# Performance work log

Hardware: AMD Instinct MI355X
Metric: run time of the kernel (lower is better)

Reference implementation:

```python
import jax, jax.numpy as jnp
import numpy as np

H = 8          # SD1.4 heads
TAU = 0.1      # HarmCfg.tau
GAMMA = 1.0    # HarmCfg.gamma
EPS = 1e-12    # F.normalize eps


def setup_inputs() -> dict:
    key = jax.random.key(0)
    ks = jax.random.split(key, 8)
    B, S, C, K, D = 16, 4096, 320, 77, 768
    return {
        "hidden_states": jax.random.normal(ks[0], (B, S, C), jnp.float32),
        "encoder_hidden_states": jax.random.normal(ks[1], (B, K, D), jnp.float32),
        "harm_vec": jax.random.normal(ks[2], (D,), jnp.float32),
        "Wq": jax.random.normal(ks[3], (C, C), jnp.float32) * 0.02,
        "Wk": jax.random.normal(ks[4], (D, C), jnp.float32) * 0.02,
        "Wv": jax.random.normal(ks[5], (D, C), jnp.float32) * 0.02,
        "Wo": jax.random.normal(ks[6], (C, C), jnp.float32) * 0.02,
        "bo": jnp.zeros((C,), jnp.float32),
    }


def reference(hidden_states, encoder_hidden_states, harm_vec, Wq, Wk, Wv, Wo, bo):
    B, S, C = hidden_states.shape
    K = encoder_hidden_states.shape[1]
    dh = C // H
    scale = 1.0 / jnp.sqrt(jnp.asarray(dh, hidden_states.dtype))

    # projections (no bias on q/k/v, as in diffusers SD1.4)
    q = (hidden_states @ Wq).reshape(B, S, H, dh)
    k = (encoder_hidden_states @ Wk).reshape(B, K, H, dh)
    v = (encoder_hidden_states @ Wv).reshape(B, K, H, dh)

    # scores: QK^T / sqrt(dh)  -> [B, H, S, K]
    scores = jnp.einsum('bqhd,bkhd->bhqk', q, k) * scale

    # cosine-similarity harmful-token penalty (broadcast over heads and queries)
    harm = harm_vec / jnp.maximum(jnp.linalg.norm(harm_vec), EPS)
    ctx_norm = encoder_hidden_states / jnp.maximum(
        jnp.linalg.norm(encoder_hidden_states, axis=-1, keepdims=True), EPS)
    cos = jnp.einsum('bkd,d->bk', ctx_norm, harm)            # [B, K]
    penalty = jnp.maximum(cos - TAU, 0.0)                     # clamp(min=0)
    scores = scores - GAMMA * penalty[:, None, None, :]

    probs = jax.nn.softmax(scores, axis=-1)                   # dropout p=0 (eval)
    out = jnp.einsum('bhqk,bkhd->bqhd', probs, v).reshape(B, S, C)
    return out @ Wo + bo
```

## Files before the change

kernel.cpp:

```cpp
#include <hip/hip_runtime.h>
#include <hip/hip_bf16.h>

#define B_ 16
#define S_ 4096
#define C_ 320
#define KK_ 77
#define D_ 768
#define H_ 8
#define DH_ 40
#define KP_ 80
#define NP_ (H_ * KP_)
#define TAU_ 0.1f
#define GAMMA_ 1.0f
#define EPS_ 1e-12f

typedef __bf16 bf16x8 __attribute__((ext_vector_type(8)));
typedef float f32x4 __attribute__((ext_vector_type(4)));
typedef unsigned short ushort8v __attribute__((ext_vector_type(8)));
typedef unsigned int u32;

#define WAITV(N)  asm volatile("s_waitcnt vmcnt(" #N ")" ::: "memory")
#define WAITVL(N) asm volatile("s_waitcnt vmcnt(" #N ") lgkmcnt(0)" ::: "memory")
#define WAITLG()  asm volatile("s_waitcnt lgkmcnt(0)" ::: "memory")
#define BAR()     __builtin_amdgcn_s_barrier()

__device__ __forceinline__ unsigned short f2bf(float f) {
    union { float f; unsigned u; } v; v.f = f;
    unsigned r = v.u + 0x7fffu + ((v.u >> 16) & 1u);
    return (unsigned short)(r >> 16);
}

__device__ __forceinline__ void gld16(const unsigned short* g, char* l) {
    __builtin_amdgcn_global_load_lds(
        (const __attribute__((address_space(1))) u32*)g,
        (__attribute__((address_space(3))) u32*)l, 16, 0, 0);
}

__global__ __launch_bounds__(256) void build_M(const float* __restrict__ Wq,
        const float* __restrict__ Wk, const float* __restrict__ Wv,
        const float* __restrict__ Wo, unsigned short* __restrict__ Bmat) {
    const int Dk = blockIdx.x * 256 + threadIdx.x;
    const int h = blockIdx.y;
    const int which = blockIdx.z >> 2;
    const int c0 = (blockIdx.z & 3) * 80;
    __shared__ float wlds[80 * 44];
    for (int i = threadIdx.x; i < 80 * DH_; i += 256) {
        int c = i / DH_, d = i % DH_;
        wlds[c * 44 + d] = which
            ? Wo[(size_t)(h * DH_ + d) * C_ + (c0 + c)]
            : Wq[(size_t)(c0 + c) * C_ + h * DH_ + d];
    }
    float a[DH_];
    const float* Arow = (which ? Wv : Wk) + (size_t)Dk * C_ + h * DH_;
    #pragma unroll
    for (int d = 0; d < DH_; ++d) a[d] = Arow[d];
    __syncthreads();
    const float scale = 0.15811388300841898f;
    for (int c = 0; c < 80; ++c) {
        float s = 0.f;
        #pragma unroll
        for (int q = 0; q < 10; ++q) {
            float4 wv4 = *(const float4*)&wlds[c * 44 + q * 4];
            s += a[q * 4 + 0] * wv4.x + a[q * 4 + 1] * wv4.y
               + a[q * 4 + 2] * wv4.z + a[q * 4 + 3] * wv4.w;
        }
        if (!which) s *= scale;
        int n = which * 2560 + h * C_ + c0 + c;
        Bmat[(size_t)n * D_ + Dk] = f2bf(s);
    }
}

__global__ __launch_bounds__(256) void prep_ehs(const float* __restrict__ ehs,
        const float* __restrict__ harm, unsigned short* __restrict__ ehs_bf,
        float* __restrict__ pen) {
    const int w = threadIdx.x >> 6, l = threadIdx.x & 63;
    const int kk = blockIdx.x * 4 + w, b = blockIdx.y;
    const size_t obase = ((size_t)b * KP_ + kk) * D_;
    if (kk >= KK_) {
        #pragma unroll
        for (int j = 0; j < 12; ++j) ehs_bf[obase + l + j * 64] = 0;
        if (l == 0) pen[b * KP_ + kk] = 0.f;
        return;
    }
    const float* er = ehs + ((size_t)b * KK_ + kk) * D_;
    float ss = 0.f, dd = 0.f, hh = 0.f;
    #pragma unroll
    for (int j = 0; j < 12; ++j) {
        float e = er[l + j * 64], hv = harm[l + j * 64];
        ehs_bf[obase + l + j * 64] = f2bf(e);
        ss += e * e; dd += e * hv; hh += hv * hv;
    }
    #pragma unroll
    for (int off = 32; off; off >>= 1) {
        ss += __shfl_xor(ss, off);
        dd += __shfl_xor(dd, off);
        hh += __shfl_xor(hh, off);
    }
    if (l == 0) {
        float cs = dd / (fmaxf(sqrtf(ss), EPS_) * fmaxf(sqrtf(hh), EPS_));
        pen[b * KP_ + kk] = GAMMA_ * fmaxf(cs - TAU_, 0.f);
    }
}

__global__ __launch_bounds__(1024) void gemm_WpU(
        const unsigned short* __restrict__ ehs_bf,
        const unsigned short* __restrict__ Bmat,
        unsigned short* __restrict__ Wp, unsigned short* __restrict__ U) {
    const int id = blockIdx.x;
    const int b = id & 15, nt = id >> 4;
    const int tid = threadIdx.x, w = tid >> 6, l = tid & 63;
    const int lrow = l & 15, lgrp = l >> 4, lk = lgrp * 8;
    __shared__ unsigned short Al[80 * 768];
    char* lds = (char*)Al;

    const unsigned short* Ag = ehs_bf + (size_t)b * KP_ * D_;
    #pragma unroll
    for (int it = 0; it < 8; ++it) {
        int ch = tid + it * 1024;
        if (ch < 7680) {
            int byte = ch * 16, row = byte / 1536;
            int a = byte ^ ((row & 7) << 4);
            *(ushort8v*)(lds + a) = *(const ushort8v*)(Ag + ch * 8);
        }
    }
    const int n0 = nt * 512 + w * 32;
    const unsigned short* Br = Bmat + (size_t)(n0 + lrow) * D_ + lk;
    bf16x8 bC[2], bN[2];
    #pragma unroll
    for (int nf = 0; nf < 2; ++nf)
        bC[nf] = *(const bf16x8*)(Br + (size_t)nf * 16 * D_);
    __syncthreads();

    f32x4 acc[5][2];
    #pragma unroll
    for (int mf = 0; mf < 5; ++mf)
        #pragma unroll
        for (int nf = 0; nf < 2; ++nf) acc[mf][nf] = (f32x4){0.f, 0.f, 0.f, 0.f};
    #pragma unroll
    for (int ks = 0; ks < D_ / 32; ++ks) {
        if (ks < D_ / 32 - 1) {
            #pragma unroll
            for (int nf = 0; nf < 2; ++nf)
                bN[nf] = *(const bf16x8*)(Br + (size_t)nf * 16 * D_ + (ks + 1) * 32);
        }
        bf16x8 af[5];
        #pragma unroll
        for (int mf = 0; mf < 5; ++mf) {
            int row = mf * 16 + lrow;
            int a = (row * 1536 + (ks * 32 + lk) * 2) ^ ((row & 7) << 4);
            af[mf] = *(const bf16x8*)(lds + a);
        }
        __builtin_amdgcn_s_setprio(1);
        #pragma unroll
        for (int mf = 0; mf < 5; ++mf)
            #pragma unroll
            for (int nf = 0; nf < 2; ++nf)
                acc[mf][nf] = __builtin_amdgcn_mfma_f32_16x16x32_bf16(
                    af[mf], bC[nf], acc[mf][nf], 0, 0, 0);
        __builtin_amdgcn_s_setprio(0);
        #pragma unroll
        for (int nf = 0; nf < 2; ++nf) bC[nf] = bN[nf];
    }
    #pragma unroll
    for (int nf = 0; nf < 2; ++nf) {
        const int col = n0 + nf * 16 + lrow;
        if (col < 2560) {
            const int h = col / C_, c = col % C_;
            #pragma unroll
            for (int mf = 0; mf < 5; ++mf)
                #pragma unroll
                for (int r = 0; r < 4; ++r) {
                    int kk = mf * 16 + lgrp * 4 + r;
                    Wp[((size_t)b * NP_ + h * KP_ + kk) * C_ + c] = f2bf(acc[mf][nf][r]);
                }
        } else {
            const int n2 = col - 2560;
            const int h = n2 / C_, c = n2 % C_;
            #pragma unroll
            for (int mf = 0; mf < 5; ++mf)
                #pragma unroll
                for (int r = 0; r < 4; ++r) {
                    int kk = mf * 16 + lgrp * 4 + r;
                    U[((size_t)b * C_ + c) * NP_ + h * KP_ + kk] = f2bf(acc[mf][nf][r]);
                }
        }
    }
}

__global__ __launch_bounds__(1024) void fused_attn(
        const float* __restrict__ hs, const unsigned short* __restrict__ Wp,
        const unsigned short* __restrict__ U, const float* __restrict__ pen,
        const float* __restrict__ bo, float* __restrict__ out) {
    const int id = blockIdx.x;
    const int xcd = id & 7, rest = id >> 3;
    const int b = xcd * 2 + (rest >> 6);
    const int s0 = (rest & 63) * 64;
    __shared__ __align__(16) char smem[122880];
    char* HS = smem;
    char* WB0 = smem + 40960;
    char* WB1 = smem + 81920;
    char* PB  = smem + 40960;
    char* UB0 = smem;
    char* UB1 = smem + 20480;
    const int tid = threadIdx.x, w = tid >> 6, l = tid & 63;
    const int lrow = l & 15, lgrp = l >> 4, lk = lgrp * 8;
    const int h = w & 7, mh = w >> 3;
    const int mgrp = w & 3, ngrp = w >> 2;

    const unsigned short* Wpb = Wp + (size_t)b * NP_ * C_;
    const unsigned short* Ub  = U  + (size_t)b * C_ * NP_;

    auto stage_wp = [&](int ks, char* buf) {
        #pragma unroll
        for (int j = 0; j < 2; ++j) {
            int L = w * 128 + j * 64 + l;
            int n = L >> 2, cs = (L & 3) ^ ((n >> 1) & 3);
            gld16(Wpb + (size_t)n * C_ + ks * 32 + cs * 8,
                  buf + (w * 128 + j * 64) * 16);
        }
        if (w < 8) {
            int L = 2048 + w * 64 + l;
            int n = L >> 2, cs = (L & 3) ^ ((n >> 1) & 3);
            gld16(Wpb + (size_t)n * C_ + ks * 32 + cs * 8,
                  buf + (2048 + w * 64) * 16);
        }
    };
    auto stage_u = [&](int ksn, char* buf) {
        {
            int L = w * 64 + l;
            int c = L >> 2, cs = (L & 3) ^ ((c >> 1) & 3);
            gld16(Ub + (size_t)c * NP_ + ksn * 32 + cs * 8, buf + (w * 64) * 16);
        }
        if (w < 4) {
            int L = 1024 + w * 64 + l;
            int c = L >> 2, cs = (L & 3) ^ ((c >> 1) & 3);
            gld16(Ub + (size_t)c * NP_ + ksn * 32 + cs * 8,
                  buf + (1024 + w * 64) * 16);
        }
    };

    float4 pv4[5];
    #pragma unroll
    for (int nf = 0; nf < 5; ++nf)
        pv4[nf] = *(const float4*)(pen + b * KP_ + nf * 16 + lgrp * 4);
    const float4* hv = (const float4*)(hs + ((size_t)b * S_ + s0) * C_);
    #pragma unroll
    for (int it = 0; it < 5; ++it) {
        int i = tid + it * 1024;
        float4 v = hv[i];
        int r = i / 80, c = (i * 4) % C_;
        ushort4 u;
        u.x = f2bf(v.x); u.y = f2bf(v.y); u.z = f2bf(v.z); u.w = f2bf(v.w);
        int a = (r * 640 + c * 2) ^ ((r & 7) << 4);
        *(ushort4*)(HS + a) = u;
    }
    #pragma unroll
    for (int nf = 0; nf < 5; ++nf)
        asm volatile("" :: "v"(pv4[nf].x), "v"(pv4[nf].y),
                           "v"(pv4[nf].z), "v"(pv4[nf].w));
    stage_wp(0, WB0);
    stage_wp(1, WB1);
    if (w < 8) { WAITVL(3); } else { WAITVL(2); }
    BAR();

    f32x4 acc[5][2];
    #pragma unroll
    for (int nf = 0; nf < 5; ++nf)
        #pragma unroll
        for (int mf = 0; mf < 2; ++mf) acc[nf][mf] = (f32x4){0.f, 0.f, 0.f, 0.f};
    #pragma unroll
    for (int ks = 0; ks < 10; ++ks) {
        char* wb = (ks & 1) ? WB1 : WB0;
        bf16x8 bC[5], hf[2];
        #pragma unroll
        for (int nf = 0; nf < 5; ++nf) {
            int n = h * KP_ + nf * 16 + lrow;
            bC[nf] = *(const bf16x8*)(wb + n * 64 + ((lgrp ^ ((n >> 1) & 3)) << 4));
        }
        #pragma unroll
        for (int mf = 0; mf < 2; ++mf) {
            int row = mh * 32 + mf * 16 + lrow;
            int a = (row * 640 + (ks * 32 + lk) * 2) ^ ((row & 7) << 4);
            hf[mf] = *(const bf16x8*)(HS + a);
        }
        __builtin_amdgcn_s_setprio(1);
        #pragma unroll
        for (int nf = 0; nf < 5; ++nf)
            #pragma unroll
            for (int mf = 0; mf < 2; ++mf)
                acc[nf][mf] = __builtin_amdgcn_mfma_f32_16x16x32_bf16(
                    bC[nf], hf[mf], acc[nf][mf], 0, 0, 0);
        __builtin_amdgcn_s_setprio(0);
        WAITLG();
        BAR();
        if (ks < 9) {
            if (ks < 8) {
                stage_wp(ks + 2, wb);
                if (w < 8) { WAITV(3); } else { WAITV(2); }
            } else {
                WAITV(0);
            }
            BAR();
        }
    }

    stage_u(0, UB0);
    stage_u(1, UB1);

    float inv2[2];
    #pragma unroll
    for (int mf = 0; mf < 2; ++mf) {
        float mx = -1e30f;
        #pragma unroll
        for (int nf = 0; nf < 5; ++nf)
            #pragma unroll
            for (int r = 0; r < 4; ++r) {
                float x = acc[nf][mf][r] - ((const float*)&pv4[nf])[r];
                if (nf == 4 && r >= 1) x = (lgrp == 3) ? -1e30f : x;
                acc[nf][mf][r] = x;
                mx = fmaxf(mx, x);
            }
        mx = fmaxf(mx, __shfl_xor(mx, 16));
        mx = fmaxf(mx, __shfl_xor(mx, 32));
        float s = 0.f;
        #pragma unroll
        for (int nf = 0; nf < 5; ++nf)
            #pragma unroll
            for (int r = 0; r < 4; ++r) {
                float e = __expf(acc[nf][mf][r] - mx);
                acc[nf][mf][r] = e; s += e;
            }
        s += __shfl_xor(s, 16);
        s += __shfl_xor(s, 32);
        inv2[mf] = 1.f / s;
    }

    #pragma unroll
    for (int mf = 0; mf < 2; ++mf) {
        const int m = mh * 32 + mf * 16 + lrow;
        const float inv = inv2[mf];
        #pragma unroll
        for (int nf = 0; nf < 5; ++nf) {
            ushort4 u;
            u.x = f2bf(acc[nf][mf][0] * inv);
            u.y = f2bf(acc[nf][mf][1] * inv);
            u.z = f2bf(acc[nf][mf][2] * inv);
            u.w = f2bf(acc[nf][mf][3] * inv);
            int a = (m * 1280 + (h * KP_ + nf * 16 + lgrp * 4) * 2) ^ ((m & 7) << 4);
            *(ushort4*)(PB + a) = u;
        }
    }
    if (w < 4) { WAITVL(2); } else { WAITVL(1); }
    BAR();

    f32x4 acc2[5];
    #pragma unroll
    for (int nf = 0; nf < 5; ++nf) acc2[nf] = (f32x4){0.f, 0.f, 0.f, 0.f};
    #pragma unroll
    for (int ksn = 0; ksn < 20; ++ksn) {
        char* ub = (ksn & 1) ? UB1 : UB0;
        bf16x8 pa, uf[5];
        {
            int row = mgrp * 16 + lrow;
            int a = (row * 1280 + (ksn * 32 + lk) * 2) ^ ((row & 7) << 4);
            pa = *(const bf16x8*)(PB + a);
        }
        #pragma unroll
        for (int nf = 0; nf < 5; ++nf) {
            int c = ngrp * KP_ + nf * 16 + lrow;
            uf[nf] = *(const bf16x8*)(ub + c * 64 + ((lgrp ^ ((c >> 1) & 3)) << 4));
        }
        __builtin_amdgcn_s_setprio(1);
        #pragma unroll
        for (int nf = 0; nf < 5; ++nf)
            acc2[nf] = __builtin_amdgcn_mfma_f32_16x16x32_bf16(pa, uf[nf], acc2[nf], 0, 0, 0);
        __builtin_amdgcn_s_setprio(0);
        WAITLG();
        BAR();
        if (ksn < 19) {
            if (ksn < 18) {
                stage_u(ksn + 2, ub);
                if (w < 4) { WAITV(2); } else { WAITV(1); }
            } else {
                WAITV(0);
            }
            BAR();
        }
    }
    float bov[5];
    #pragma unroll
    for (int nf = 0; nf < 5; ++nf) bov[nf] = bo[ngrp * KP_ + nf * 16 + lrow];
    float* op = out + ((size_t)b * S_ + s0) * C_;
    #pragma unroll
    for (int r = 0; r < 4; ++r)
        #pragma unroll
        for (int nf = 0; nf < 5; ++nf)
            op[(size_t)(mgrp * 16 + lgrp * 4 + r) * C_ +
               ngrp * KP_ + nf * 16 + lrow] = acc2[nf][r] + bov[nf];
}

extern "C" void kernel_launch(void* const* d_in, const int* in_sizes, int n_in,
                              void* d_out, int out_size, void* d_ws, size_t ws_size,
                              hipStream_t stream) {
    const float* hs   = (const float*)d_in[0];
    const float* ehs  = (const float*)d_in[1];
    const float* harm = (const float*)d_in[2];
    const float* Wq   = (const float*)d_in[3];
    const float* Wk   = (const float*)d_in[4];
    const float* Wv   = (const float*)d_in[5];
    const float* Wo   = (const float*)d_in[6];
    const float* bo   = (const float*)d_in[7];
    float* out = (float*)d_out;

    char* ws = (char*)d_ws;
    unsigned short* ehs_bf = (unsigned short*)(ws);
    unsigned short* Bmat   = (unsigned short*)(ws + 1966080);
    float*          pen    = (float*)        (ws + 9830400);
    unsigned short* Wp     = (unsigned short*)(ws + 9835520);
    unsigned short* U      = (unsigned short*)(ws + 16389120);

    build_M <<<dim3(3, 8, 8),  256, 0, stream>>>(Wq, Wk, Wv, Wo, Bmat);
    prep_ehs<<<dim3(20, 16),   256, 0, stream>>>(ehs, harm, ehs_bf, pen);
    gemm_WpU<<<dim3(160),     1024, 0, stream>>>(ehs_bf, Bmat, Wp, U);
    fused_attn<<<dim3(1024),  1024, 0, stream>>>(hs, Wp, U, pen, bo, out);
}
```

Measured before the change: 175.4 us.

## Triple-buffer weight staging and split P·U GEMM into two half-K phases

Shared memory grows to 160KB, which gives three staging buffers in place of two. Both GEMM loops now prefetch three k-steps ahead. Each next-stage load is issued right after the LDS fragment reads and the barrier, so it overlaps the MFMAs, where before it waited until after the compute. The second GEMM uses 64-wide K tiles in two halves: probabilities for heads 0-3 are written into the freed HS region first, then heads 4-7. This aims to hide more global-load latency and to halve the barrier count in the second GEMM, at the cost of more LDS per block and more complex wait-count bookkeeping.

```diff
diff --git a/kernel.cpp b/kernel.cpp
--- a/kernel.cpp
+++ b/kernel.cpp
@@ -195,13 +195,11 @@
     const int xcd = id & 7, rest = id >> 3;
     const int b = xcd * 2 + (rest >> 6);
     const int s0 = (rest & 63) * 64;
-    __shared__ __align__(16) char smem[122880];
-    char* HS = smem;
-    char* WB0 = smem + 40960;
-    char* WB1 = smem + 81920;
-    char* PB  = smem + 40960;
-    char* UB0 = smem;
-    char* UB1 = smem + 20480;
+    __shared__ __align__(16) char smem[163840];
+    char* HS  = smem;
+    char* BUF0 = smem + 40960;
+    char* BUF1 = smem + 81920;
+    char* BUF2 = smem + 122880;
     const int tid = threadIdx.x, w = tid >> 6, l = tid & 63;
     const int lrow = l & 15, lgrp = l >> 4, lk = lgrp * 8;
     const int h = w & 7, mh = w >> 3;
@@ -225,20 +223,26 @@
                   buf + (2048 + w * 64) * 16);
         }
     };
-    auto stage_u = [&](int ksn, char* buf) {
-        {
-            int L = w * 64 + l;
-            int c = L >> 2, cs = (L & 3) ^ ((c >> 1) & 3);
-            gld16(Ub + (size_t)c * NP_ + ksn * 32 + cs * 8, buf + (w * 64) * 16);
-        }
-        if (w < 4) {
-            int L = 1024 + w * 64 + l;
-            int c = L >> 2, cs = (L & 3) ^ ((c >> 1) & 3);
-            gld16(Ub + (size_t)c * NP_ + ksn * 32 + cs * 8,
-                  buf + (1024 + w * 64) * 16);
+    auto stage_u = [&](int p, int t, char* buf) {
+        const int k0 = p * 320 + t * 64;
+        #pragma unroll
+        for (int j = 0; j < 2; ++j) {
+            int L = w * 128 + j * 64 + l;
+            int c = L >> 3, s2 = (L & 7) ^ (c & 7);
+            gld16(Ub + (size_t)c * NP_ + k0 + s2 * 8,
+                  buf + (w * 128 + j * 64) * 16);
+        }
+        if (w < 8) {
+            int L = 2048 + w * 64 + l;
+            int c = L >> 3, s2 = (L & 7) ^ (c & 7);
+            gld16(Ub + (size_t)c * NP_ + k0 + s2 * 8,
+                  buf + (2048 + w * 64) * 16);
         }
     };
 
+    stage_wp(0, BUF0);
+    stage_wp(1, BUF1);
+    stage_wp(2, BUF2);
     float4 pv4[5];
     #pragma unroll
     for (int nf = 0; nf < 5; ++nf)
@@ -258,9 +262,7 @@
     for (int nf = 0; nf < 5; ++nf)
         asm volatile("" :: "v"(pv4[nf].x), "v"(pv4[nf].y),
                            "v"(pv4[nf].z), "v"(pv4[nf].w));
-    stage_wp(0, WB0);
-    stage_wp(1, WB1);
-    if (w < 8) { WAITVL(3); } else { WAITVL(2); }
+    if (w < 8) { WAITVL(6); } else { WAITVL(4); }
     BAR();
 
     f32x4 acc[5][2];
@@ -270,7 +272,7 @@
         for (int mf = 0; mf < 2; ++mf) acc[nf][mf] = (f32x4){0.f, 0.f, 0.f, 0.f};
     #pragma unroll
     for (int ks = 0; ks < 10; ++ks) {
-        char* wb = (ks & 1) ? WB1 : WB0;
+        char* wb = (ks % 3 == 0) ? BUF0 : (ks % 3 == 1) ? BUF1 : BUF2;
         bf16x8 bC[5], hf[2];
         #pragma unroll
         for (int nf = 0; nf < 5; ++nf) {
@@ -283,6 +285,9 @@
             int a = (row * 640 + (ks * 32 + lk) * 2) ^ ((row & 7) << 4);
             hf[mf] = *(const bf16x8*)(HS + a);
         }
+        WAITLG();
+        BAR();
+        if (ks < 7) stage_wp(ks + 3, wb);
         __builtin_amdgcn_s_setprio(1);
         #pragma unroll
         for (int nf = 0; nf < 5; ++nf)
@@ -291,21 +296,17 @@
                 acc[nf][mf] = __builtin_amdgcn_mfma_f32_16x16x32_bf16(
                     bC[nf], hf[mf], acc[nf][mf], 0, 0, 0);
         __builtin_amdgcn_s_setprio(0);
-        WAITLG();
-        BAR();
         if (ks < 9) {
-            if (ks < 8) {
-                stage_wp(ks + 2, wb);
-                if (w < 8) { WAITV(3); } else { WAITV(2); }
-            } else {
-                WAITV(0);
-            }
+            if (ks < 7)      { if (w < 8) { WAITV(6); } else { WAITV(4); } }
+            else if (ks == 7){ if (w < 8) { WAITV(3); } else { WAITV(2); } }
+            else             { WAITV(0); }
             BAR();
         }
     }
 
-    stage_u(0, UB0);
-    stage_u(1, UB1);
+    stage_u(0, 0, BUF0);
+    stage_u(0, 1, BUF1);
+    stage_u(0, 2, BUF2);
 
     float inv2[2];
     #pragma unroll
@@ -334,59 +335,94 @@
         s += __shfl_xor(s, 32);
         inv2[mf] = 1.f / s;
     }
-
-    #pragma unroll
-    for (int mf = 0; mf < 2; ++mf) {
-        const int m = mh * 32 + mf * 16 + lrow;
-        const float inv = inv2[mf];
+    ushort4 pk[2][5];
+    #pragma unroll
+    for (int mf = 0; mf < 2; ++mf)
         #pragma unroll
         for (int nf = 0; nf < 5; ++nf) {
-            ushort4 u;
-            u.x = f2bf(acc[nf][mf][0] * inv);
-            u.y = f2bf(acc[nf][mf][1] * inv);
-            u.z = f2bf(acc[nf][mf][2] * inv);
-            u.w = f2bf(acc[nf][mf][3] * inv);
-            int a = (m * 1280 + (h * KP_ + nf * 16 + lgrp * 4) * 2) ^ ((m & 7) << 4);
-            *(ushort4*)(PB + a) = u;
-        }
-    }
-    if (w < 4) { WAITVL(2); } else { WAITVL(1); }
+            pk[mf][nf].x = f2bf(acc[nf][mf][0] * inv2[mf]);
+            pk[mf][nf].y = f2bf(acc[nf][mf][1] * inv2[mf]);
+            pk[mf][nf].z = f2bf(acc[nf][mf][2] * inv2[mf]);
+            pk[mf][nf].w = f2bf(acc[nf][mf][3] * inv2[mf]);
+        }
+    if ((h >> 2) == 0) {
+        #pragma unroll
+        for (int mf = 0; mf < 2; ++mf) {
+            int m = mh * 32 + mf * 16 + lrow;
+            #pragma unroll
+            for (int nf = 0; nf < 5; ++nf) {
+                int col = (h & 3) * KP_ + nf * 16 + lgrp * 4;
+                *(ushort4*)(HS + ((m * 640 + col * 2) ^ ((m & 7) << 4))) = pk[mf][nf];
+            }
+        }
+    }
+    if (w < 8) { WAITVL(6); } else { WAITVL(4); }
     BAR();
 
     f32x4 acc2[5];
     #pragma unroll
     for (int nf = 0; nf < 5; ++nf) acc2[nf] = (f32x4){0.f, 0.f, 0.f, 0.f};
     #pragma unroll
-    for (int ksn = 0; ksn < 20; ++ksn) {
-        char* ub = (ksn & 1) ? UB1 : UB0;
-        bf16x8 pa, uf[5];
-        {
-            int row = mgrp * 16 + lrow;
-            int a = (row * 1280 + (ksn * 32 + lk) * 2) ^ ((row & 7) << 4);
-            pa = *(const bf16x8*)(PB + a);
-        }
-        #pragma unroll
-        for (int nf = 0; nf < 5; ++nf) {
-            int c = ngrp * KP_ + nf * 16 + lrow;
-            uf[nf] = *(const bf16x8*)(ub + c * 64 + ((lgrp ^ ((c >> 1) & 3)) << 4));
-        }
-        __builtin_amdgcn_s_setprio(1);
-        #pragma unroll
-        for (int nf = 0; nf < 5; ++nf)
-            acc2[nf] = __builtin_amdgcn_mfma_f32_16x16x32_bf16(pa, uf[nf], acc2[nf], 0, 0, 0);
-        __builtin_amdgcn_s_setprio(0);
-        WAITLG();
-        BAR();
-        if (ksn < 19) {
-            if (ksn < 18) {
-                stage_u(ksn + 2, ub);
-                if (w < 4) { WAITV(2); } else { WAITV(1); }
-            } else {
-                WAITV(0);
-            }
+    for (int p = 0; p < 2; ++p) {
+        #pragma unroll
+        for (int t = 0; t < 5; ++t) {
+            char* ub = (t % 3 == 0) ? BUF0 : (t % 3 == 1) ? BUF1 : BUF2;
+            bf16x8 pa[2], uf[5][2];
+            #pragma unroll
+            for (int ks2 = 0; ks2 < 2; ++ks2) {
+                int m = mgrp * 16 + lrow;
+                int abyte = (m * 640 + (t * 64 + ks2 * 32 + lgrp * 8) * 2)
+                            ^ ((m & 7) << 4);
+                pa[ks2] = *(const bf16x8*)(HS + abyte);
+            }
+            #pragma unroll
+            for (int nf = 0; nf < 5; ++nf) {
+                int c = ngrp * KP_ + nf * 16 + lrow;
+                #pragma unroll
+                for (int ks2 = 0; ks2 < 2; ++ks2) {
+                    int s2 = (ks2 * 4 + lgrp) ^ (c & 7);
+                    uf[nf][ks2] = *(const bf16x8*)(ub + c * 128 + s2 * 16);
+                }
+            }
+            WAITLG();
             BAR();
-        }
-    }
+            if (t < 2) stage_u(p, t + 3, ub);
+            __builtin_amdgcn_s_setprio(1);
+            #pragma unroll
+            for (int nf = 0; nf < 5; ++nf)
+                #pragma unroll
+                for (int ks2 = 0; ks2 < 2; ++ks2)
+                    acc2[nf] = __builtin_amdgcn_mfma_f32_16x16x32_bf16(
+                        pa[ks2], uf[nf][ks2], acc2[nf], 0, 0, 0);
+            __builtin_amdgcn_s_setprio(0);
+            if (p == 1 && t == 4) break;
+            if (t < 4) {
+                if (t < 2)       { if (w < 8) { WAITV(6); } else { WAITV(4); } }
+                else if (t == 2) { if (w < 8) { WAITV(3); } else { WAITV(2); } }
+                else             { WAITV(0); }
+                BAR();
+            }
+        }
+        if (p == 0) {
+            stage_u(1, 0, BUF0);
+            stage_u(1, 1, BUF1);
+            stage_u(1, 2, BUF2);
+            if ((h >> 2) == 1) {
+                #pragma unroll
+                for (int mf = 0; mf < 2; ++mf) {
+                    int m = mh * 32 + mf * 16 + lrow;
+                    #pragma unroll
+                    for (int nf = 0; nf < 5; ++nf) {
+                        int col = (h & 3) * KP_ + nf * 16 + lgrp * 4;
+                        *(ushort4*)(HS + ((m * 640 + col * 2) ^ ((m & 7) << 4))) = pk[mf][nf];
+                    }
+                }
+            }
+            if (w < 8) { WAITVL(6); } else { WAITVL(4); }
+            BAR();
+        }
+    }
+
     float bov[5];
     #pragma unroll
     for (int nf = 0; nf < 5; ++nf) bov[nf] = bo[ngrp * KP_ + nf * 16 + lrow];
```

Result: slower. 200.0 us (+14.0%).

## Deepen LDS pipelines to triple/quad buffering and issue prefetch before MFMAs

Applied to the files above, without the earlier changes.

Grows shared memory to 160KB so the Wp stage uses three buffers and the U stage uses four. The first Wp loads are issued before the hidden-state conversion, and each iteration's prefetch is issued right after its fragments are read into registers, before the MFMAs. This hides more global-load latency behind compute. The cost is more LDS use, though the block already runs one per CU, and more complex vmcnt bookkeeping.

```diff
diff --git a/kernel.cpp b/kernel.cpp
--- a/kernel.cpp
+++ b/kernel.cpp
@@ -195,13 +195,15 @@
     const int xcd = id & 7, rest = id >> 3;
     const int b = xcd * 2 + (rest >> 6);
     const int s0 = (rest & 63) * 64;
-    __shared__ __align__(16) char smem[122880];
-    char* HS = smem;
+    __shared__ __align__(16) char smem[163840];
+    char* HS  = smem;
     char* WB0 = smem + 40960;
     char* WB1 = smem + 81920;
+    char* WB2 = smem + 122880;
     char* PB  = smem + 40960;
-    char* UB0 = smem;
-    char* UB1 = smem + 20480;
+    char* UB[4];
+    UB[0] = smem;          UB[1] = smem + 20480;
+    UB[2] = smem + 122880; UB[3] = smem + 143360;
     const int tid = threadIdx.x, w = tid >> 6, l = tid & 63;
     const int lrow = l & 15, lgrp = l >> 4, lk = lgrp * 8;
     const int h = w & 7, mh = w >> 3;
@@ -239,6 +241,9 @@
         }
     };
 
+    stage_wp(0, WB0);
+    stage_wp(1, WB1);
+    stage_wp(2, WB2);
     float4 pv4[5];
     #pragma unroll
     for (int nf = 0; nf < 5; ++nf)
@@ -258,9 +263,7 @@
     for (int nf = 0; nf < 5; ++nf)
         asm volatile("" :: "v"(pv4[nf].x), "v"(pv4[nf].y),
                            "v"(pv4[nf].z), "v"(pv4[nf].w));
-    stage_wp(0, WB0);
-    stage_wp(1, WB1);
-    if (w < 8) { WAITVL(3); } else { WAITVL(2); }
+    if (w < 8) { WAITVL(6); } else { WAITVL(4); }
     BAR();
 
     f32x4 acc[5][2];
@@ -270,7 +273,7 @@
         for (int mf = 0; mf < 2; ++mf) acc[nf][mf] = (f32x4){0.f, 0.f, 0.f, 0.f};
     #pragma unroll
     for (int ks = 0; ks < 10; ++ks) {
-        char* wb = (ks & 1) ? WB1 : WB0;
+        char* wb = (ks % 3 == 0) ? WB0 : (ks % 3 == 1) ? WB1 : WB2;
         bf16x8 bC[5], hf[2];
         #pragma unroll
         for (int nf = 0; nf < 5; ++nf) {
@@ -283,6 +286,9 @@
             int a = (row * 640 + (ks * 32 + lk) * 2) ^ ((row & 7) << 4);
             hf[mf] = *(const bf16x8*)(HS + a);
         }
+        WAITLG();
+        BAR();
+        if (ks < 7) stage_wp(ks + 3, wb);
         __builtin_amdgcn_s_setprio(1);
         #pragma unroll
         for (int nf = 0; nf < 5; ++nf)
@@ -291,21 +297,18 @@
                 acc[nf][mf] = __builtin_amdgcn_mfma_f32_16x16x32_bf16(
                     bC[nf], hf[mf], acc[nf][mf], 0, 0, 0);
         __builtin_amdgcn_s_setprio(0);
-        WAITLG();
-        BAR();
         if (ks < 9) {
-            if (ks < 8) {
-                stage_wp(ks + 2, wb);
-                if (w < 8) { WAITV(3); } else { WAITV(2); }
-            } else {
-                WAITV(0);
-            }
+            if (ks < 7)      { if (w < 8) { WAITV(6); } else { WAITV(4); } }
+            else if (ks == 7){ if (w < 8) { WAITV(3); } else { WAITV(2); } }
+            else             { WAITV(0); }
             BAR();
         }
     }
 
-    stage_u(0, UB0);
-    stage_u(1, UB1);
+    stage_u(0, UB[0]);
+    stage_u(1, UB[1]);
+    stage_u(2, UB[2]);
+    stage_u(3, UB[3]);
 
     float inv2[2];
     #pragma unroll
@@ -350,19 +353,19 @@
             *(ushort4*)(PB + a) = u;
         }
     }
-    if (w < 4) { WAITVL(2); } else { WAITVL(1); }
+    if (w < 4) { WAITVL(6); } else { WAITVL(3); }
     BAR();
 
     f32x4 acc2[5];
     #pragma unroll
     for (int nf = 0; nf < 5; ++nf) acc2[nf] = (f32x4){0.f, 0.f, 0.f, 0.f};
     #pragma unroll
-    for (int ksn = 0; ksn < 20; ++ksn) {
-        char* ub = (ksn & 1) ? UB1 : UB0;
+    for (int t = 0; t < 20; ++t) {
+        char* ub = UB[t & 3];
         bf16x8 pa, uf[5];
         {
-            int row = mgrp * 16 + lrow;
-            int a = (row * 1280 + (ksn * 32 + lk) * 2) ^ ((row & 7) << 4);
+            int m = mgrp * 16 + lrow;
+            int a = (m * 1280 + (t * 32 + lk) * 2) ^ ((m & 7) << 4);
             pa = *(const bf16x8*)(PB + a);
         }
         #pragma unroll
@@ -370,23 +373,23 @@
             int c = ngrp * KP_ + nf * 16 + lrow;
             uf[nf] = *(const bf16x8*)(ub + c * 64 + ((lgrp ^ ((c >> 1) & 3)) << 4));
         }
+        WAITLG();
+        BAR();
+        if (t < 16) stage_u(t + 4, ub);
         __builtin_amdgcn_s_setprio(1);
         #pragma unroll
         for (int nf = 0; nf < 5; ++nf)
             acc2[nf] = __builtin_amdgcn_mfma_f32_16x16x32_bf16(pa, uf[nf], acc2[nf], 0, 0, 0);
         __builtin_amdgcn_s_setprio(0);
-        WAITLG();
-        BAR();
-        if (ksn < 19) {
-            if (ksn < 18) {
-                stage_u(ksn + 2, ub);
-                if (w < 4) { WAITV(2); } else { WAITV(1); }
-            } else {
-                WAITV(0);
-            }
+        if (t < 19) {
+            if (t < 16)       { if (w < 4) { WAITV(6); } else { WAITV(3); } }
+            else if (t == 16) { if (w < 4) { WAITV(4); } else { WAITV(2); } }
+            else if (t == 17) { if (w < 4) { WAITV(2); } else { WAITV(1); } }
+            else              { WAITV(0); }
             BAR();
         }
     }
+
     float bov[5];
     #pragma unroll
     for (int nf = 0; nf < 5; ++nf) bov[nf] = bo[ngrp * KP_ + nf * 16 + lrow];
```

New measurement: 173.6 us. About the same (-1.0%).

## Halve attention tile to 32 rows, 512 threads, triple-buffered Wp staging

Applied to the files above, without the earlier changes.

The fused attention kernel now handles 32 query rows per block with 8 waves (one per head) instead of 64 rows with 16 waves. Grid size doubles and shared memory drops to 80KB, which should allow more blocks per CU. Wp staging becomes a three-slot ring of 16-column slices with a new unswizzled layout, and loads for both loops are now issued before the MFMAs so they overlap with compute. The catch is that each block streams the per-batch Wp and U matrices for only half as many rows, doubling global/L2 traffic for those weights.

```diff
diff --git a/kernel.cpp b/kernel.cpp
--- a/kernel.cpp
+++ b/kernel.cpp
@@ -187,101 +187,116 @@
     }
 }
 
-__global__ __launch_bounds__(1024) void fused_attn(
+__global__ __launch_bounds__(512, 4) void fused_attn(
         const float* __restrict__ hs, const unsigned short* __restrict__ Wp,
         const unsigned short* __restrict__ U, const float* __restrict__ pen,
         const float* __restrict__ bo, float* __restrict__ out) {
     const int id = blockIdx.x;
     const int xcd = id & 7, rest = id >> 3;
-    const int b = xcd * 2 + (rest >> 6);
-    const int s0 = (rest & 63) * 64;
-    __shared__ __align__(16) char smem[122880];
-    char* HS = smem;
-    char* WB0 = smem + 40960;
-    char* WB1 = smem + 81920;
-    char* PB  = smem + 40960;
-    char* UB0 = smem;
-    char* UB1 = smem + 20480;
+    const int b = xcd * 2 + (rest >> 7);
+    const int s0 = (rest & 127) * 32;
+    __shared__ __align__(16) char smem[81920];
+    char* HS  = smem;
+    char* PB  = smem;
+    char* WH0 = smem + 20480;
+    char* WH1 = smem + 40960;
+    char* WH2 = smem + 61440;
+    char* UB0 = smem + 40960;
+    char* UB1 = smem + 61440;
     const int tid = threadIdx.x, w = tid >> 6, l = tid & 63;
     const int lrow = l & 15, lgrp = l >> 4, lk = lgrp * 8;
-    const int h = w & 7, mh = w >> 3;
-    const int mgrp = w & 3, ngrp = w >> 2;
+    const int h = w;
+    const int mgrp = w & 1, ngrp = w >> 1;
 
     const unsigned short* Wpb = Wp + (size_t)b * NP_ * C_;
     const unsigned short* Ub  = U  + (size_t)b * C_ * NP_;
 
-    auto stage_wp = [&](int ks, char* buf) {
-        #pragma unroll
-        for (int j = 0; j < 2; ++j) {
-            int L = w * 128 + j * 64 + l;
-            int n = L >> 2, cs = (L & 3) ^ ((n >> 1) & 3);
-            gld16(Wpb + (size_t)n * C_ + ks * 32 + cs * 8,
-                  buf + (w * 128 + j * 64) * 16);
-        }
-        if (w < 8) {
-            int L = 2048 + w * 64 + l;
-            int n = L >> 2, cs = (L & 3) ^ ((n >> 1) & 3);
-            gld16(Wpb + (size_t)n * C_ + ks * 32 + cs * 8,
-                  buf + (2048 + w * 64) * 16);
+    auto stage_wh = [&](int hh, char* buf) {
+        if (w < 4) {
+            #pragma unroll
+            for (int j = 0; j < 3; ++j) {
+                int L0 = w * 192 + j * 64;
+                int L = L0 + l;
+                int c8 = L / 640, n = L % 640;
+                gld16(Wpb + (size_t)n * C_ + hh * 16 + c8 * 8, buf + L0 * 16);
+            }
+        } else {
+            #pragma unroll
+            for (int j = 0; j < 2; ++j) {
+                int L0 = 768 + (w - 4) * 128 + j * 64;
+                int L = L0 + l;
+                int c8 = L / 640, n = L % 640;
+                gld16(Wpb + (size_t)n * C_ + hh * 16 + c8 * 8, buf + L0 * 16);
+            }
         }
     };
     auto stage_u = [&](int ksn, char* buf) {
-        {
-            int L = w * 64 + l;
-            int c = L >> 2, cs = (L & 3) ^ ((c >> 1) & 3);
-            gld16(Ub + (size_t)c * NP_ + ksn * 32 + cs * 8, buf + (w * 64) * 16);
-        }
         if (w < 4) {
-            int L = 1024 + w * 64 + l;
-            int c = L >> 2, cs = (L & 3) ^ ((c >> 1) & 3);
-            gld16(Ub + (size_t)c * NP_ + ksn * 32 + cs * 8,
-                  buf + (1024 + w * 64) * 16);
+            #pragma unroll
+            for (int j = 0; j < 3; ++j) {
+                int L0 = w * 192 + j * 64;
+                int L = L0 + l;
+                int c = L >> 2, cs = (L & 3) ^ ((c >> 1) & 3);
+                gld16(Ub + (size_t)c * NP_ + ksn * 32 + cs * 8, buf + L0 * 16);
+            }
+        } else {
+            #pragma unroll
+            for (int j = 0; j < 2; ++j) {
+                int L0 = 768 + (w - 4) * 128 + j * 64;
+                int L = L0 + l;
+                int c = L >> 2, cs = (L & 3) ^ ((c >> 1) & 3);
+                gld16(Ub + (size_t)c * NP_ + ksn * 32 + cs * 8, buf + L0 * 16);
+            }
         }
     };
 
-    float4 pv4[5];
-    #pragma unroll
-    for (int nf = 0; nf < 5; ++nf)
-        pv4[nf] = *(const float4*)(pen + b * KP_ + nf * 16 + lgrp * 4);
     const float4* hv = (const float4*)(hs + ((size_t)b * S_ + s0) * C_);
+    float4 hvv[5];
+    #pragma unroll
+    for (int it = 0; it < 5; ++it) hvv[it] = hv[tid + it * 512];
+    stage_wh(0, WH0);
+    stage_wh(1, WH1);
+    stage_wh(2, WH2);
     #pragma unroll
     for (int it = 0; it < 5; ++it) {
-        int i = tid + it * 1024;
-        float4 v = hv[i];
+        int i = tid + it * 512;
         int r = i / 80, c = (i * 4) % C_;
         ushort4 u;
-        u.x = f2bf(v.x); u.y = f2bf(v.y); u.z = f2bf(v.z); u.w = f2bf(v.w);
+        u.x = f2bf(hvv[it].x); u.y = f2bf(hvv[it].y);
+        u.z = f2bf(hvv[it].z); u.w = f2bf(hvv[it].w);
         int a = (r * 640 + c * 2) ^ ((r & 7) << 4);
         *(ushort4*)(HS + a) = u;
     }
+    if (w < 4) { WAITVL(3); } else { WAITVL(2); }
+    BAR();
+
+    f32x4 acc[5][2];
     #pragma unroll
     for (int nf = 0; nf < 5; ++nf)
-        asm volatile("" :: "v"(pv4[nf].x), "v"(pv4[nf].y),
-                           "v"(pv4[nf].z), "v"(pv4[nf].w));
-    stage_wp(0, WB0);
-    stage_wp(1, WB1);
-    if (w < 8) { WAITVL(3); } else { WAITVL(2); }
-    BAR();
-
-    f32x4 acc[5][2];
-    #pragma unroll
-    for (int nf = 0; nf < 5; ++nf)
         #pragma unroll
         for (int mf = 0; mf < 2; ++mf) acc[nf][mf] = (f32x4){0.f, 0.f, 0.f, 0.f};
     #pragma unroll
     for (int ks = 0; ks < 10; ++ks) {
-        char* wb = (ks & 1) ? WB1 : WB0;
         bf16x8 bC[5], hf[2];
         #pragma unroll
         for (int nf = 0; nf < 5; ++nf) {
             int n = h * KP_ + nf * 16 + lrow;
-            bC[nf] = *(const bf16x8*)(wb + n * 64 + ((lgrp ^ ((n >> 1) & 3)) << 4));
+            int hb = (2 * ks + (lgrp >> 1)) % 3;
+            char* base = (hb == 0) ? WH0 : (hb == 1) ? WH1 : WH2;
+            bC[nf] = *(const bf16x8*)(base + (lgrp & 1) * 10240 + n * 16);
         }
         #pragma unroll
         for (int mf = 0; mf < 2; ++mf) {
-            int row = mh * 32 + mf * 16 + lrow;
+            int row = mf * 16 + lrow;
             int a = (row * 640 + (ks * 32 + lk) * 2) ^ ((row & 7) << 4);
             hf[mf] = *(const bf16x8*)(HS + a);
+        }
+        WAITLG();
+        BAR();
+        {
+            int h3 = 2 * ks + 3, h4 = 2 * ks + 4;
+            if (h3 <= 19) stage_wh(h3, (h3 % 3 == 0) ? WH0 : (h3 % 3 == 1) ? WH1 : WH2);
+            if (h4 <= 19) stage_wh(h4, (h4 % 3 == 0) ? WH0 : (h4 % 3 == 1) ? WH1 : WH2);
         }
         __builtin_amdgcn_s_setprio(1);
         #pragma unroll
@@ -291,19 +306,21 @@
                 acc[nf][mf] = __builtin_amdgcn_mfma_f32_16x16x32_bf16(
                     bC[nf], hf[mf], acc[nf][mf], 0, 0, 0);
         __builtin_amdgcn_s_setprio(0);
-        WAITLG();
-        BAR();
         if (ks < 9) {
-            if (ks < 8) {
-                stage_wp(ks + 2, wb);
-                if (w < 8) { WAITV(3); } else { WAITV(2); }
-            } else {
-                WAITV(0);
-            }
+            if (ks <= 7) { if (w < 4) { WAITV(3); } else { WAITV(2); } }
+            else         { WAITV(0); }
             BAR();
         }
     }
 
+    float4 pv4[5];
+    #pragma unroll
+    for (int nf = 0; nf < 5; ++nf)
+        pv4[nf] = *(const float4*)(pen + b * KP_ + nf * 16 + lgrp * 4);
+    #pragma unroll
+    for (int nf = 0; nf < 5; ++nf)
+        asm volatile("" :: "v"(pv4[nf].x), "v"(pv4[nf].y),
+                           "v"(pv4[nf].z), "v"(pv4[nf].w));
     stage_u(0, UB0);
     stage_u(1, UB1);
 
@@ -337,7 +354,7 @@
 
     #pragma unroll
     for (int mf = 0; mf < 2; ++mf) {
-        const int m = mh * 32 + mf * 16 + lrow;
+        const int m = mf * 16 + lrow;
         const float inv = inv2[mf];
         #pragma unroll
         for (int nf = 0; nf < 5; ++nf) {
@@ -350,19 +367,19 @@
             *(ushort4*)(PB + a) = u;
         }
     }
-    if (w < 4) { WAITVL(2); } else { WAITVL(1); }
+    if (w < 4) { WAITVL(3); } else { WAITVL(2); }
     BAR();
 
     f32x4 acc2[5];
     #pragma unroll
     for (int nf = 0; nf < 5; ++nf) acc2[nf] = (f32x4){0.f, 0.f, 0.f, 0.f};
     #pragma unroll
-    for (int ksn = 0; ksn < 20; ++ksn) {
-        char* ub = (ksn & 1) ? UB1 : UB0;
+    for (int t = 0; t < 20; ++t) {
+        char* ub = (t & 1) ? UB1 : UB0;
         bf16x8 pa, uf[5];
         {
-            int row = mgrp * 16 + lrow;
-            int a = (row * 1280 + (ksn * 32 + lk) * 2) ^ ((row & 7) << 4);
+            int m = mgrp * 16 + lrow;
+            int a = (m * 1280 + (t * 32 + lk) * 2) ^ ((m & 7) << 4);
             pa = *(const bf16x8*)(PB + a);
         }
         #pragma unroll
@@ -370,23 +387,21 @@
             int c = ngrp * KP_ + nf * 16 + lrow;
             uf[nf] = *(const bf16x8*)(ub + c * 64 + ((lgrp ^ ((c >> 1) & 3)) << 4));
         }
+        WAITLG();
+        BAR();
+        if (t < 18) stage_u(t + 2, ub);
         __builtin_amdgcn_s_setprio(1);
         #pragma unroll
         for (int nf = 0; nf < 5; ++nf)
             acc2[nf] = __builtin_amdgcn_mfma_f32_16x16x32_bf16(pa, uf[nf], acc2[nf], 0, 0, 0);
         __builtin_amdgcn_s_setprio(0);
-        WAITLG();
-        BAR();
-        if (ksn < 19) {
-            if (ksn < 18) {
-                stage_u(ksn + 2, ub);
-                if (w < 4) { WAITV(2); } else { WAITV(1); }
-            } else {
-                WAITV(0);
-            }
+        if (t < 19) {
+            if (t < 18) { if (w < 4) { WAITV(3); } else { WAITV(2); } }
+            else        { WAITV(0); }
             BAR();
         }
     }
+
     float bov[5];
     #pragma unroll
     for (int nf = 0; nf < 5; ++nf) bov[nf] = bo[ngrp * KP_ + nf * 16 + lrow];
@@ -422,5 +437,5 @@
     build_M <<<dim3(3, 8, 8),  256, 0, stream>>>(Wq, Wk, Wv, Wo, Bmat);
     prep_ehs<<<dim3(20, 16),   256, 0, stream>>>(ehs, harm, ehs_bf, pen);
     gemm_WpU<<<dim3(160),     1024, 0, stream>>>(ehs_bf, Bmat, Wp, U);
-    fused_attn<<<dim3(1024),  1024, 0, stream>>>(hs, Wp, U, pen, bo, out);
-}
+    fused_attn<<<dim3(2048),   512, 0, stream>>>(hs, Wp, U, pen, bo, out);
+}
```

After: 328.4 us. 87.3% more time.
